# Kernel tuning notes

Hardware: AMD Instinct MI355X
Metric: run time of the kernel (lower is better)

The kernel has to match this reference:

```python
import jax, jax.numpy as jnp
import numpy as np

HEADS = 4
ATTN_MODE = 'strided'
LOCAL_ATTN_CTX = 32
BLOCKSIZE = 32


def strided_transpose(x, n_ctx, local_attn_ctx):
    # [n, t, e] -> [n, bT_ctx, local, e] -> [n, local, bT_ctx, e] -> [n, t, e]
    bT_ctx = n_ctx // local_attn_ctx
    n, t, e = x.shape
    x = x.reshape(n, bT_ctx, local_attn_ctx, e)
    x = jnp.transpose(x, (0, 2, 1, 3))
    return x.reshape(n, t, e)


def setup_inputs() -> dict:
    key = jax.random.key(0)
    kq, kk, kv = jax.random.split(key, 3)
    shape = (2, 4096, 1024)
    return {
        'q': jax.random.normal(kq, shape, dtype=jnp.float32),
        'k': jax.random.normal(kk, shape, dtype=jnp.float32),
        'v': jax.random.normal(kv, shape, dtype=jnp.float32),
    }


def reference(q, k, v):
    n_ctx = q.shape[1]
    if ATTN_MODE == 'strided':
        bT_ctx = n_ctx // LOCAL_ATTN_CTX
        assert bT_ctx % BLOCKSIZE == 0
        q = strided_transpose(q, n_ctx, LOCAL_ATTN_CTX)
        k = strided_transpose(k, n_ctx, LOCAL_ATTN_CTX)
        v = strided_transpose(v, n_ctx, LOCAL_ATTN_CTX)
    n_state = q.shape[-1] // HEADS
    scale = 1.0 / np.sqrt(n_state)
    w = jnp.einsum('nte,nse->nts', q, k)            # [n, t, t] full scores
    w = jax.nn.softmax(w * scale, axis=-1)
    a = jnp.einsum('nts,nse->nte', w, v)
    if ATTN_MODE == 'strided':
        n, t, e = a.shape
        bT_ctx = n_ctx // LOCAL_ATTN_CTX
        a = a.reshape(n, LOCAL_ATTN_CTX, bT_ctx, e)
        a = jnp.transpose(a, (0, 2, 1, 3))
        a = a.reshape(n, t, e)
    return a
```

## Files before the change

kernel.cpp:

```cpp
#include <hip/hip_runtime.h>

using short8  = __attribute__((ext_vector_type(8))) short;
using ushort8 = __attribute__((ext_vector_type(8))) unsigned short;
using f32x4   = __attribute__((ext_vector_type(4))) float;

#define T 4096
#define E 1024
#define NB 2

__device__ __forceinline__ unsigned short f2bf(float f) {
    unsigned int u = __builtin_bit_cast(unsigned int, f);
    u = (u + 0x7FFFu + ((u >> 16) & 1u)) >> 16;
    return (unsigned short)u;
}

__device__ __forceinline__ void gld16(const unsigned short* g, unsigned short* l) {
    __builtin_amdgcn_global_load_lds(
        (__attribute__((address_space(1))) void*)g,
        (__attribute__((address_space(3))) void*)l, 16, 0, 0);
}

__device__ __forceinline__ void do_cvt(const float* __restrict__ src,
                                       unsigned short* __restrict__ dst, int blk) {
    size_t i = ((size_t)blk * 256 + threadIdx.x) * 8;
    float4 f0 = *(const float4*)(src + i);
    float4 f1 = *(const float4*)(src + i + 4);
    ushort8 u;
    u[0]=f2bf(f0.x); u[1]=f2bf(f0.y); u[2]=f2bf(f0.z); u[3]=f2bf(f0.w);
    u[4]=f2bf(f1.x); u[5]=f2bf(f1.y); u[6]=f2bf(f1.z); u[7]=f2bf(f1.w);
    *(ushort8*)(dst + i) = u;
}

__device__ __forceinline__ void do_vt(const float* __restrict__ v,
                                      unsigned short* __restrict__ vt, int id,
                                      float (*tile)[65]) {
    int b   = id / (64 * 16);
    int rem = id % (64 * 16);
    int t0  = (rem / 16) * 64;
    int e0  = (rem % 16) * 64;
    int tid = threadIdx.x;
    int r   = tid >> 2;
    int c0  = (tid & 3) * 16;
    const float* src = v + ((size_t)(b * T + t0 + r)) * E + e0 + c0;
    #pragma unroll
    for (int i = 0; i < 4; i++) {
        float4 f = *(const float4*)(src + i * 4);
        tile[r][c0 + i*4 + 0] = f.x;
        tile[r][c0 + i*4 + 1] = f.y;
        tile[r][c0 + i*4 + 2] = f.z;
        tile[r][c0 + i*4 + 3] = f.w;
    }
    __syncthreads();
    int er = tid >> 2;
    #pragma unroll
    for (int ch = 0; ch < 2; ch++) {
        int tl = (tid & 3) * 16 + ch * 8;
        ushort8 u;
        #pragma unroll
        for (int j = 0; j < 8; j++) u[j] = f2bf(tile[tl + j][er]);
        *(ushort8*)(vt + ((size_t)(b * E + e0 + er)) * T + t0 + tl) = u;
    }
}

__global__ __launch_bounds__(256) void prep(const float* __restrict__ q,
                                            const float* __restrict__ k,
                                            const float* __restrict__ v,
                                            unsigned short* __restrict__ qb,
                                            unsigned short* __restrict__ kb,
                                            unsigned short* __restrict__ vt,
                                            float* __restrict__ lsum) {
    __shared__ float tile[64][65];
    int bid = blockIdx.x;
    if (bid < 4096)        do_cvt(q, qb, bid);
    else if (bid < 8192)   do_cvt(k, kb, bid - 4096);
    else if (bid < 10240)  do_vt(v, vt, bid - 8192, tile);
    else                   lsum[(bid - 10240) * 256 + threadIdx.x] = 0.0f;
}

__global__ __launch_bounds__(256) void prologue(const float* __restrict__ q,
                                                const float* __restrict__ k,
                                                unsigned short* __restrict__ qb,
                                                unsigned short* __restrict__ kb,
                                                float* __restrict__ lsum) {
    int bid = blockIdx.x;
    if (bid < 4096)      do_cvt(q, qb, bid);
    else if (bid < 8192) do_cvt(k, kb, bid - 4096);
    else                 lsum[(bid - 8192) * 256 + threadIdx.x] = 0.0f;
}
__global__ __launch_bounds__(256) void v_transpose(const float* __restrict__ v,
                                                   unsigned short* __restrict__ vt) {
    __shared__ float tile[64][65];
    do_vt(v, vt, blockIdx.x, tile);
}

template <int KITERS>
__device__ __forceinline__ void gemm_core64(const unsigned short* Abase, int apitch,
                                            const unsigned short* Bbase, int bpitch,
                                            unsigned short* ldsA, unsigned short* ldsB,
                                            int tid, f32x4 (&acc)[4][4]) {
    constexpr int TILE64 = 128 * 64;
    const int lane = tid & 63, wave = tid >> 6;
    const int l15 = lane & 15, kq = lane >> 4;
    const int wm = (wave & 1) * 64, wn = (wave >> 1) * 64;

    int goA[4], goB[4], lo[4];
    #pragma unroll
    for (int i = 0; i < 4; i++) {
        int p = i * 256 + tid;
        int r = p >> 3, c = p & 7;
        int sw = c ^ (r & 7);
        goA[i] = r * apitch + sw * 8;
        goB[i] = r * bpitch + sw * 8;
        lo[i] = (i * 256 + wave * 64) * 8;
    }
    int aoff[2][4], boff[2][4];
    #pragma unroll
    for (int mi = 0; mi < 4; mi++) {
        int r = wm + mi * 16 + l15;
        aoff[0][mi] = (r * 8 + (kq ^ (r & 7))) * 8;
        aoff[1][mi] = (r * 8 + ((kq ^ 4) ^ (r & 7))) * 8;
        int rn = wn + mi * 16 + l15;
        boff[0][mi] = (rn * 8 + (kq ^ (rn & 7))) * 8;
        boff[1][mi] = (rn * 8 + ((kq ^ 4) ^ (rn & 7))) * 8;
    }

    #pragma unroll
    for (int i = 0; i < 4; i++) gld16(Abase + goA[i], ldsA + lo[i]);
    #pragma unroll
    for (int i = 0; i < 4; i++) gld16(Bbase + goB[i], ldsB + lo[i]);

    int cbuf = 0;
    for (int kt = 0; kt < KITERS; kt++) {
        int pk = (kt + 1 < KITERS) ? (kt + 1) : 0;
        int ob = cbuf ^ 1;
        asm volatile("s_barrier" ::: "memory");
        #pragma unroll
        for (int i = 0; i < 4; i++) gld16(Abase + goA[i] + pk * 64, ldsA + ob * TILE64 + lo[i]);
        #pragma unroll
        for (int i = 0; i < 4; i++) gld16(Bbase + goB[i] + pk * 64, ldsB + ob * TILE64 + lo[i]);
        asm volatile("s_waitcnt vmcnt(8)" ::: "memory");
        asm volatile("s_barrier" ::: "memory");

        const unsigned short* A = ldsA + cbuf * TILE64;
        const unsigned short* B = ldsB + cbuf * TILE64;
        #pragma unroll
        for (int ks = 0; ks < 2; ks++) {
            short8 af[4], bf[4];
            #pragma unroll
            for (int i = 0; i < 4; i++) {
                af[i] = *(const short8*)(A + aoff[ks][i]);
                bf[i] = *(const short8*)(B + boff[ks][i]);
            }
            #pragma unroll
            for (int mi = 0; mi < 4; mi++)
                #pragma unroll
                for (int ni = 0; ni < 4; ni++)
                    acc[mi][ni] = __builtin_amdgcn_mfma_f32_16x16x32_bf16(af[mi], bf[ni], acc[mi][ni], 0, 0, 0);
        }
        cbuf = ob;
    }
}

__global__ __launch_bounds__(256, 2) void pass1(const unsigned short* __restrict__ qb,
                                                const unsigned short* __restrict__ kb,
                                                unsigned short* __restrict__ P,
                                                float* __restrict__ lsum) {
    constexpr int TILE64 = 128 * 64;
    __shared__ unsigned short ldsA[2 * TILE64];
    __shared__ unsigned short ldsB[2 * TILE64];

    const int bx  = blockIdx.x;
    const int xc  = bx & 7;
    const int sj  = bx >> 3;
    const int gm  = xc * 8 + (sj & 7);
    const int nt  = ((sj >> 6) << 3) + ((sj >> 3) & 7);
    const int b   = gm >> 5, mt = gm & 31;
    const int tid = threadIdx.x;

    f32x4 acc[4][4];
    #pragma unroll
    for (int i = 0; i < 4; i++)
        #pragma unroll
        for (int jj = 0; jj < 4; jj++) acc[i][jj] = {};

    gemm_core64<E / 64>(qb + ((size_t)b * T + mt * 128) * E, E,
                        kb + ((size_t)b * T + nt * 128) * E, E,
                        ldsA, ldsB, tid, acc);

    const int lane = tid & 63, wave = tid >> 6;
    const int wm = (wave & 1) * 64, wn = (wave >> 1) * 64;
    const int quad = lane >> 4, l15 = lane & 15;
    const float sl2 = 0.0625f * 1.44269504089f;
    const int col0 = nt * 128 + wn + l15;

    #pragma unroll
    for (int mi = 0; mi < 4; mi++) {
        #pragma unroll
        for (int r = 0; r < 4; r++) {
            int row = mt * 128 + wm + mi * 16 + quad * 4 + r;
            size_t base = ((size_t)b * T + row) * T + col0;
            float rs = 0.0f;
            #pragma unroll
            for (int ni = 0; ni < 4; ni++) {
                float p = exp2f(acc[mi][ni][r] * sl2 - 12.0f);
                P[base + ni * 16] = f2bf(p);
                rs += p;
            }
            rs += __shfl_xor(rs, 1);
            rs += __shfl_xor(rs, 2);
            rs += __shfl_xor(rs, 4);
            rs += __shfl_xor(rs, 8);
            if (l15 == 0) atomicAdd(lsum + b * T + row, rs);
        }
    }
}

__global__ __launch_bounds__(256, 2) void pass2(const unsigned short* __restrict__ P,
                                                const unsigned short* __restrict__ vt,
                                                const float* __restrict__ lsum,
                                                float* __restrict__ out) {
    constexpr int TILE64 = 128 * 64;
    __shared__ unsigned short ldsA[2 * TILE64];
    __shared__ unsigned short ldsB[2 * TILE64];

    const int bx = blockIdx.x;
    const int xc = bx & 7, j = bx >> 3;
    const int gm = xc * 8 + (j & 7);
    const int nt = j >> 3;
    const int b = gm >> 5, mt = gm & 31;
    const int tid = threadIdx.x;

    f32x4 acc[4][4];
    #pragma unroll
    for (int i = 0; i < 4; i++)
        #pragma unroll
        for (int jj = 0; jj < 4; jj++) acc[i][jj] = {};

    gemm_core64<T / 64>(P + ((size_t)b * T + mt * 128) * T, T,
                        vt + ((size_t)b * E + nt * 128) * T, T,
                        ldsA, ldsB, tid, acc);

    const int lane = tid & 63, wave = tid >> 6;
    const int wm = (wave & 1) * 64, wn = (wave >> 1) * 64;
    const int quad = lane >> 4, l15 = lane & 15;
    const int col0 = nt * 128 + wn + l15;

    #pragma unroll
    for (int mi = 0; mi < 4; mi++) {
        #pragma unroll
        for (int r = 0; r < 4; r++) {
            int row = mt * 128 + wm + mi * 16 + quad * 4 + r;
            float rl = 1.0f / lsum[b * T + row];
            size_t base = ((size_t)b * T + row) * E + col0;
            #pragma unroll
            for (int ni = 0; ni < 4; ni++)
                out[base + ni * 16] = acc[mi][ni][r] * rl;
        }
    }
}

extern "C" void kernel_launch(void* const* d_in, const int* in_sizes, int n_in,
                              void* d_out, int out_size, void* d_ws, size_t ws_size,
                              hipStream_t stream) {
    const float* q = (const float*)d_in[0];
    const float* k = (const float*)d_in[1];
    const float* v = (const float*)d_in[2];
    float* out = (float*)d_out;

    const size_t QK = (size_t)NB * T * E;
    const size_t PSZ = (size_t)NB * T * T;
    float* lsum = (float*)d_ws;
    unsigned short* qbw = (unsigned short*)((char*)d_ws + 32768);
    unsigned short* kbw = qbw + QK;
    unsigned short* Pw  = kbw + QK;

    const size_t full_need = 32768 + (3 * QK + PSZ) * sizeof(unsigned short);

    if (ws_size >= full_need) {
        unsigned short* vtw = Pw + PSZ;
        prep<<<10272, 256, 0, stream>>>(q, k, v, qbw, kbw, vtw, lsum);
        pass1<<<2048, 256, 0, stream>>>(qbw, kbw, Pw, lsum);
        pass2<<<512, 256, 0, stream>>>(Pw, vtw, lsum, out);
    } else {
        unsigned short* vtw = qbw;
        prologue<<<8224, 256, 0, stream>>>(q, k, qbw, kbw, lsum);
        pass1<<<2048, 256, 0, stream>>>(qbw, kbw, Pw, lsum);
        v_transpose<<<NB * 64 * 16, 256, 0, stream>>>(v, vtw);
        pass2<<<512, 256, 0, stream>>>(Pw, vtw, lsum, out);
    }
}
```

Baseline: 297.2 us.

## Make pass1 blocks compute four N-tiles with continuous cross-tile prefetch

Each pass1 workgroup now processes four consecutive 128-column key tiles, reusing the same Q rows, and runs one double-buffered load pipeline across all four tiles, so the prefetch of the next tile overlaps the epilogue of the current one. The grid shrinks from 2048 to 512 blocks. The goal is to cut per-block launch and pipeline prologue/drain costs and to overlap the exp/store epilogue with loads. In exchange there are fewer blocks (512 across 256 CUs at 2 per CU, roughly one wave of work) and a longer serial chain per block, which risks tail imbalance. The Q tile is still reloaded from global memory for each key tile.

```diff
diff --git a/kernel.cpp b/kernel.cpp
--- a/kernel.cpp
+++ b/kernel.cpp
@@ -173,9 +173,37 @@
     const int xc  = bx & 7;
     const int sj  = bx >> 3;
     const int gm  = xc * 8 + (sj & 7);
-    const int nt  = ((sj >> 6) << 3) + ((sj >> 3) & 7);
-    const int b   = gm >> 5, mt = gm & 31;
+    const int ntb = (sj >> 3) * 4;
+    const int b = gm >> 5, mt = gm & 31;
     const int tid = threadIdx.x;
+    const int lane = tid & 63, wave = tid >> 6;
+    const int l15 = lane & 15, kq = lane >> 4;
+    const int wm = (wave & 1) * 64, wn = (wave >> 1) * 64;
+    const int quad = lane >> 4;
+
+    const unsigned short* Ab = qb + ((size_t)b * T + mt * 128) * E;
+    const unsigned short* Bb = kb + ((size_t)b * T + ntb * 128) * E;
+
+    int goA[4], goB[4], lo[4];
+    #pragma unroll
+    for (int i = 0; i < 4; i++) {
+        int p = i * 256 + tid;
+        int r = p >> 3, c = p & 7;
+        int sw = c ^ (r & 7);
+        goA[i] = r * E + sw * 8;
+        goB[i] = r * E + sw * 8;
+        lo[i] = (i * 256 + wave * 64) * 8;
+    }
+    int aoff[2][4], boff[2][4];
+    #pragma unroll
+    for (int mi = 0; mi < 4; mi++) {
+        int r = wm + mi * 16 + l15;
+        aoff[0][mi] = (r * 8 + (kq ^ (r & 7))) * 8;
+        aoff[1][mi] = (r * 8 + ((kq ^ 4) ^ (r & 7))) * 8;
+        int rn = wn + mi * 16 + l15;
+        boff[0][mi] = (rn * 8 + (kq ^ (rn & 7))) * 8;
+        boff[1][mi] = (rn * 8 + ((kq ^ 4) ^ (rn & 7))) * 8;
+    }
 
     f32x4 acc[4][4];
     #pragma unroll
@@ -183,35 +211,77 @@
         #pragma unroll
         for (int jj = 0; jj < 4; jj++) acc[i][jj] = {};
 
-    gemm_core64<E / 64>(qb + ((size_t)b * T + mt * 128) * E, E,
-                        kb + ((size_t)b * T + nt * 128) * E, E,
-                        ldsA, ldsB, tid, acc);
-
-    const int lane = tid & 63, wave = tid >> 6;
-    const int wm = (wave & 1) * 64, wn = (wave >> 1) * 64;
-    const int quad = lane >> 4, l15 = lane & 15;
+    #pragma unroll
+    for (int i = 0; i < 4; i++) gld16(Ab + goA[i], ldsA + lo[i]);
+    #pragma unroll
+    for (int i = 0; i < 4; i++) gld16(Bb + goB[i], ldsB + lo[i]);
+
     const float sl2 = 0.0625f * 1.44269504089f;
-    const int col0 = nt * 128 + wn + l15;
-
-    #pragma unroll
-    for (int mi = 0; mi < 4; mi++) {
-        #pragma unroll
-        for (int r = 0; r < 4; r++) {
-            int row = mt * 128 + wm + mi * 16 + quad * 4 + r;
-            size_t base = ((size_t)b * T + row) * T + col0;
-            float rs = 0.0f;
-            #pragma unroll
-            for (int ni = 0; ni < 4; ni++) {
-                float p = exp2f(acc[mi][ni][r] * sl2 - 12.0f);
-                P[base + ni * 16] = f2bf(p);
-                rs += p;
+    int cbuf = 0;
+    for (int it = 0; it < 4; ++it) {
+        for (int kt = 0; kt < 16; ++kt) {
+            const int ob = cbuf ^ 1;
+            asm volatile("s_barrier" ::: "memory");
+            int nit = it, nk = kt + 1;
+            if (nk == 16) { nk = 0; nit++; }
+            if (nit < 4) {
+                const unsigned short* An = Ab + nk * 64;
+                const unsigned short* Bn = Bb + (size_t)nit * (128 * E) + nk * 64;
+                #pragma unroll
+                for (int i = 0; i < 4; i++) gld16(An + goA[i], ldsA + ob * TILE64 + lo[i]);
+                #pragma unroll
+                for (int i = 0; i < 4; i++) gld16(Bn + goB[i], ldsB + ob * TILE64 + lo[i]);
+                asm volatile("s_waitcnt vmcnt(8)" ::: "memory");
+            } else {
+                asm volatile("s_waitcnt vmcnt(0)" ::: "memory");
             }
-            rs += __shfl_xor(rs, 1);
-            rs += __shfl_xor(rs, 2);
-            rs += __shfl_xor(rs, 4);
-            rs += __shfl_xor(rs, 8);
-            if (l15 == 0) atomicAdd(lsum + b * T + row, rs);
+            asm volatile("s_barrier" ::: "memory");
+
+            const unsigned short* A = ldsA + cbuf * TILE64;
+            const unsigned short* B = ldsB + cbuf * TILE64;
+            #pragma unroll
+            for (int ks = 0; ks < 2; ks++) {
+                short8 af[4], bf[4];
+                #pragma unroll
+                for (int i = 0; i < 4; i++) {
+                    af[i] = *(const short8*)(A + aoff[ks][i]);
+                    bf[i] = *(const short8*)(B + boff[ks][i]);
+                }
+                #pragma unroll
+                for (int mi = 0; mi < 4; mi++)
+                    #pragma unroll
+                    for (int ni = 0; ni < 4; ni++)
+                        acc[mi][ni] = __builtin_amdgcn_mfma_f32_16x16x32_bf16(af[mi], bf[ni], acc[mi][ni], 0, 0, 0);
+            }
+            cbuf = ob;
         }
+
+        const int nt = ntb + it;
+        const int col0 = nt * 128 + wn + l15;
+        #pragma unroll
+        for (int mi = 0; mi < 4; mi++) {
+            #pragma unroll
+            for (int r = 0; r < 4; r++) {
+                int row = mt * 128 + wm + mi * 16 + quad * 4 + r;
+                size_t base = ((size_t)b * T + row) * T + col0;
+                float rs = 0.0f;
+                #pragma unroll
+                for (int ni = 0; ni < 4; ni++) {
+                    float p = exp2f(acc[mi][ni][r] * sl2 - 12.0f);
+                    P[base + ni * 16] = f2bf(p);
+                    rs += p;
+                }
+                rs += __shfl_xor(rs, 1);
+                rs += __shfl_xor(rs, 2);
+                rs += __shfl_xor(rs, 4);
+                rs += __shfl_xor(rs, 8);
+                if (l15 == 0) atomicAdd(lsum + b * T + row, rs);
+            }
+        }
+        #pragma unroll
+        for (int i = 0; i < 4; i++)
+            #pragma unroll
+            for (int jj = 0; jj < 4; jj++) acc[i][jj] = {};
     }
 }
 
@@ -279,12 +349,12 @@
     if (ws_size >= full_need) {
         unsigned short* vtw = Pw + PSZ;
         prep<<<10272, 256, 0, stream>>>(q, k, v, qbw, kbw, vtw, lsum);
-        pass1<<<2048, 256, 0, stream>>>(qbw, kbw, Pw, lsum);
+        pass1<<<512, 256, 0, stream>>>(qbw, kbw, Pw, lsum);
         pass2<<<512, 256, 0, stream>>>(Pw, vtw, lsum, out);
     } else {
         unsigned short* vtw = qbw;
         prologue<<<8224, 256, 0, stream>>>(q, k, qbw, kbw, lsum);
-        pass1<<<2048, 256, 0, stream>>>(qbw, kbw, Pw, lsum);
+        pass1<<<512, 256, 0, stream>>>(qbw, kbw, Pw, lsum);
         v_transpose<<<NB * 64 * 16, 256, 0, stream>>>(v, vtw);
         pass2<<<512, 256, 0, stream>>>(Pw, vtw, lsum, out);
     }
```

Measured after the change: 302.6 us. Within noise of the previous version (+1.8%).
